# Kernel optimization log

Hardware: AMD Instinct MI355X
Metric: run time of the kernel (lower is better)

The kernel has to match this reference:

```python
import jax, jax.numpy as jnp
import numpy as np

N_NODES = 100000
HIDDEN = 128
E = 524288  # edges per graph (pos and neg)


def setup_inputs() -> dict:
    key = jax.random.key(0)
    ks = jax.random.split(key, 8)
    return {
        "z_src": jax.random.normal(ks[0], (N_NODES, HIDDEN), dtype=jnp.float32),
        "z_dst": jax.random.normal(ks[1], (N_NODES, HIDDEN), dtype=jnp.float32),
        "pos_src": jax.random.randint(ks[2], (E,), 0, N_NODES, dtype=jnp.int64),
        "pos_dst": jax.random.randint(ks[3], (E,), 0, N_NODES, dtype=jnp.int64),
        "neg_src": jax.random.randint(ks[4], (E,), 0, N_NODES, dtype=jnp.int64),
        "neg_dst": jax.random.randint(ks[5], (E,), 0, N_NODES, dtype=jnp.int64),
        "W1": jax.random.normal(ks[6], (2 * HIDDEN, HIDDEN), dtype=jnp.float32) * (1.0 / np.sqrt(2 * HIDDEN)),
        "b1": jnp.zeros((HIDDEN,), dtype=jnp.float32),
        "W2": jax.random.normal(ks[7], (HIDDEN, 1), dtype=jnp.float32) * (1.0 / np.sqrt(HIDDEN)),
        "b2": jnp.zeros((1,), dtype=jnp.float32),
    }


def reference(z_src, z_dst, pos_src, pos_dst, neg_src, neg_dst, W1, b1, W2, b2):
    # Gather endpoint features for pos then neg edges (cat along edge dim)
    src_idx = jnp.concatenate([pos_src, neg_src])  # [2E]
    dst_idx = jnp.concatenate([pos_dst, neg_dst])  # [2E]
    z = jnp.concatenate([z_src[src_idx], z_dst[dst_idx]], axis=-1)  # [2E, 2h]
    z = jax.nn.relu(z @ W1 + b1)  # [2E, h]
    z = z @ W2 + b2               # [2E, 1]
    return z.reshape(-1)
```

## Files before the change

kernel.cpp:

```cpp
#include <hip/hip_runtime.h>
#include <hip/hip_bf16.h>
#include <cstdint>

#define N_NODES 100000
#define HIDDEN  128
#define NEDGE   524288
#define NT      6250
#define PBLK    256
#define WSTRIDE (PBLK * 4)

typedef __attribute__((ext_vector_type(8))) short short8;
typedef __attribute__((ext_vector_type(4))) float f32x4;

__device__ __forceinline__ unsigned short f2b(float f) {
    unsigned u = __float_as_uint(f);
    u += 0x7FFFu + ((u >> 16) & 1u);
    return (unsigned short)(u >> 16);
}
__device__ __forceinline__ float b2f(unsigned x16) {
    return __uint_as_float(x16 << 16);
}

__device__ __forceinline__ void async_copy16(const float* g, float* l) {
    __builtin_amdgcn_global_load_lds(
        (const __attribute__((address_space(1))) unsigned int*)g,
        (__attribute__((address_space(3))) unsigned int*)l,
        16, 0, 0);
}

__global__ void wp_kernel(const float* __restrict__ W1,
                          unsigned short* __restrict__ Wp)
{
    const int f = blockIdx.x;
    const int tb = blockIdx.y;
    const int lane = threadIdx.x;
    const int t = lane & 15, q = lane >> 4;
    const int n = f >> 2, ks = f & 3;
    short8 v;
#pragma unroll
    for (int j = 0; j < 8; ++j)
        v[j] = (short)f2b(W1[(size_t)(tb * 128 + ks * 32 + q * 8 + j) * 128 + n * 16 + t]);
    *(short8*)(Wp + ((size_t)(tb * 32 + f) * 64 + lane) * 8) = v;
}

__global__ __launch_bounds__(256, 2)
void precompute_kernel(const float* __restrict__ z_src,
                       const float* __restrict__ z_dst,
                       const unsigned short* __restrict__ Wp,
                       const float* __restrict__ b1,
                       unsigned short* __restrict__ Asrc,
                       unsigned short* __restrict__ Adst)
{
    const int table = blockIdx.y;
    const float* __restrict__ z = table ? z_dst : z_src;
    unsigned short* __restrict__ A = table ? Adst : Asrc;

    __shared__ float zbuf[4][2][2048];

    const int tid = threadIdx.x;
    const int wave = tid >> 6;
    const int lane = tid & 63;
    const int t = lane & 15;
    const int q = lane >> 4;

    short8 wfrag[32];
    {
        const unsigned short* wp = Wp + ((size_t)table * 32 * 64 + lane) * 8;
#pragma unroll
        for (int f = 0; f < 32; ++f)
            wfrag[f] = *(const short8*)(wp + (size_t)f * 64 * 8);
    }

    float4 b1v[8];
#pragma unroll
    for (int n = 0; n < 8; ++n)
        b1v[n] = (table == 0) ? *(const float4*)(b1 + n * 16 + q * 4)
                              : make_float4(0.f, 0.f, 0.f, 0.f);

    const int lhi = lane >> 5;
    const int llo = lane & 31;
#define STAGE(m0, p)                                                          \
    do {                                                                      \
        _Pragma("unroll")                                                     \
        for (int j = 0; j < 8; ++j) {                                         \
            const int r = j * 2 + lhi;                                        \
            const int c = llo ^ (r & 7);                                      \
            async_copy16(z + (size_t)((m0) + r) * 128 + c * 4,                \
                         &zbuf[wave][p][j * 256]);                            \
        }                                                                     \
    } while (0)

    int tile = blockIdx.x * 4 + wave;
    int p = 0;
    STAGE(tile * 16, 0);
    __builtin_amdgcn_s_waitcnt(0xF70);
    asm volatile("" ::: "memory");

    while (tile < NT) {
        const int m0 = tile * 16;
        const int ntile = tile + WSTRIDE;
        const int nm0 = (ntile < NT ? ntile : tile) * 16;
        STAGE(nm0, p ^ 1);
        asm volatile("" ::: "memory");
        __builtin_amdgcn_s_waitcnt(0xF78);
        asm volatile("" ::: "memory");

        short8 b[4];
#pragma unroll
        for (int ks = 0; ks < 4; ++ks) {
            const int c0 = ks * 8 + 2 * q;
            const int s = t & 7;
            const float4 v0 = *(const float4*)&zbuf[wave][p][(t * 32 + (c0 ^ s)) * 4];
            const float4 v1 = *(const float4*)&zbuf[wave][p][(t * 32 + ((c0 + 1) ^ s)) * 4];
            b[ks][0] = (short)f2b(v0.x); b[ks][1] = (short)f2b(v0.y);
            b[ks][2] = (short)f2b(v0.z); b[ks][3] = (short)f2b(v0.w);
            b[ks][4] = (short)f2b(v1.x); b[ks][5] = (short)f2b(v1.y);
            b[ks][6] = (short)f2b(v1.z); b[ks][7] = (short)f2b(v1.w);
        }

        f32x4 acc[8];
#pragma unroll
        for (int n = 0; n < 8; ++n) acc[n] = (f32x4){0.f, 0.f, 0.f, 0.f};
#pragma unroll
        for (int n = 0; n < 8; ++n)
#pragma unroll
            for (int ks = 0; ks < 4; ++ks)
                acc[n] = __builtin_amdgcn_mfma_f32_16x16x32_bf16(
                             wfrag[n * 4 + ks], b[ks], acc[n], 0, 0, 0);

        unsigned short* ob = (unsigned short*)&zbuf[wave][p][0];
        const int sw = (t & 7) * 2;
#pragma unroll
        for (int n = 0; n < 8; ++n) {
            ushort4 h;
            h.x = f2b(acc[n][0] + b1v[n].x);
            h.y = f2b(acc[n][1] + b1v[n].y);
            h.z = f2b(acc[n][2] + b1v[n].z);
            h.w = f2b(acc[n][3] + b1v[n].w);
            *(ushort4*)&ob[t * 136 + (((n * 4 + q) ^ sw) * 4)] = h;
        }
        const int rr = lane >> 4;
#pragma unroll
        for (int it = 0; it < 4; ++it) {
            const int r = it * 4 + rr;
            const uint4 v = *(const uint4*)&ob[r * 136 + (((2 * t) ^ ((r & 7) * 2)) * 4)];
            *(uint4*)(A + (size_t)(m0 + r) * 128 + t * 8) = v;
        }
        asm volatile("" ::: "memory");

        p ^= 1;
        tile = ntile;
    }
#undef STAGE
}

__global__ __launch_bounds__(256, 6)
void edge_kernel(const unsigned short* __restrict__ Asrc,
                 const unsigned short* __restrict__ Adst,
                 const int* __restrict__ pos_src,
                 const int* __restrict__ pos_dst,
                 const int* __restrict__ neg_src,
                 const int* __restrict__ neg_dst,
                 const float* __restrict__ W2,
                 const float* __restrict__ b2,
                 float* __restrict__ out)
{
    const int tid = threadIdx.x;
    const int t = tid & 15;
    const int g = tid >> 4;

    const bool is_pos = blockIdx.x < 4096;
    const int* __restrict__ sp = is_pos ? pos_src : neg_src;
    const int* __restrict__ dp = is_pos ? pos_dst : neg_dst;
    const int eb = (is_pos ? (int)blockIdx.x : (int)blockIdx.x - 4096) * 128;

    float w2r[8];
#pragma unroll
    for (int j = 0; j < 8; ++j) w2r[j] = W2[t * 8 + j];
    const float bias2 = b2[0];

    int sidx[8], didx[8];
#pragma unroll
    for (int i = 0; i < 8; ++i) {
        sidx[i] = sp[eb + i * 16 + g];
        didx[i] = dp[eb + i * 16 + g];
    }

    uint4 ua[2][2], ub[2][2];
#pragma unroll
    for (int k = 0; k < 2; ++k) {
        ua[0][k] = *(const uint4*)(Asrc + (size_t)sidx[k] * 128 + t * 8);
        ub[0][k] = *(const uint4*)(Adst + (size_t)didx[k] * 128 + t * 8);
    }
    asm volatile("" ::: "memory");

#pragma unroll
    for (int c = 0; c < 4; ++c) {
        if (c < 3) {
#pragma unroll
            for (int k = 0; k < 2; ++k) {
                ua[(c + 1) & 1][k] =
                    *(const uint4*)(Asrc + (size_t)sidx[(c + 1) * 2 + k] * 128 + t * 8);
                ub[(c + 1) & 1][k] =
                    *(const uint4*)(Adst + (size_t)didx[(c + 1) * 2 + k] * 128 + t * 8);
            }
        }
        asm volatile("" ::: "memory");
#pragma unroll
        for (int k = 0; k < 2; ++k) {
            const unsigned* pa = (const unsigned*)&ua[c & 1][k];
            const unsigned* pb = (const unsigned*)&ub[c & 1][k];
            float acc = 0.f;
#pragma unroll
            for (int j2 = 0; j2 < 4; ++j2) {
                float h0 = b2f(pa[j2] & 0xFFFFu) + b2f(pb[j2] & 0xFFFFu);
                float h1 = b2f(pa[j2] >> 16)     + b2f(pb[j2] >> 16);
                h0 = fmaxf(h0, 0.f);
                h1 = fmaxf(h1, 0.f);
                acc = fmaf(h0, w2r[2 * j2], acc);
                acc = fmaf(h1, w2r[2 * j2 + 1], acc);
            }
            acc += __shfl_xor(acc, 1);
            acc += __shfl_xor(acc, 2);
            acc += __shfl_xor(acc, 4);
            acc += __shfl_xor(acc, 8);
            if (t == 0) out[blockIdx.x * 128 + (c * 2 + k) * 16 + g] = acc + bias2;
        }
    }
}

extern "C" void kernel_launch(void* const* d_in, const int* in_sizes, int n_in,
                              void* d_out, int out_size, void* d_ws, size_t ws_size,
                              hipStream_t stream) {
    const float* z_src  = (const float*)d_in[0];
    const float* z_dst  = (const float*)d_in[1];
    const int* pos_src  = (const int*)d_in[2];
    const int* pos_dst  = (const int*)d_in[3];
    const int* neg_src  = (const int*)d_in[4];
    const int* neg_dst  = (const int*)d_in[5];
    const float* W1     = (const float*)d_in[6];
    const float* b1     = (const float*)d_in[7];
    const float* W2     = (const float*)d_in[8];
    const float* b2     = (const float*)d_in[9];
    float* out = (float*)d_out;

    unsigned short* Asrc = (unsigned short*)d_ws;
    unsigned short* Adst = Asrc + (size_t)N_NODES * HIDDEN;
    unsigned short* Wp   = Adst + (size_t)N_NODES * HIDDEN;

    wp_kernel<<<dim3(32, 2), 64, 0, stream>>>(W1, Wp);

    precompute_kernel<<<dim3(PBLK, 2), 256, 0, stream>>>(z_src, z_dst, Wp, b1,
                                                         Asrc, Adst);

    edge_kernel<<<8192, 256, 0, stream>>>(Asrc, Adst, pos_src, pos_dst,
                                          neg_src, neg_dst, W2, b2, out);
}
```

Measured before the change: 219.9 us.

## Issue all edge gathers upfront with staged waitcnt and halve edges per block

The edge kernel now handles 64 edges per block instead of 128, doubling the grid. Each thread issues all four gather loads at once using 32-bit byte offsets and then consumes them in order with explicit vmcnt waits, replacing the two-deep double buffer. The launch bounds occupancy hint rises from 6 to 7. The goal is more memory-level parallelism and cheaper address arithmetic for the random row gathers, at the cost of more blocks and repeated W2 loads per block.

```diff
diff --git a/kernel.cpp b/kernel.cpp
--- a/kernel.cpp
+++ b/kernel.cpp
@@ -154,7 +154,7 @@
 #undef STAGE
 }
 
-__global__ __launch_bounds__(256, 6)
+__global__ __launch_bounds__(256, 7)
 void edge_kernel(const unsigned short* __restrict__ Asrc,
                  const unsigned short* __restrict__ Adst,
                  const int* __restrict__ pos_src,
@@ -169,64 +169,62 @@
     const int t = tid & 15;
     const int g = tid >> 4;
 
-    const bool is_pos = blockIdx.x < 4096;
+    const bool is_pos = blockIdx.x < 8192;
     const int* __restrict__ sp = is_pos ? pos_src : neg_src;
     const int* __restrict__ dp = is_pos ? pos_dst : neg_dst;
-    const int eb = (is_pos ? (int)blockIdx.x : (int)blockIdx.x - 4096) * 128;
+    const int eb = (is_pos ? (int)blockIdx.x : (int)blockIdx.x - 8192) * 64;
 
     float w2r[8];
 #pragma unroll
     for (int j = 0; j < 8; ++j) w2r[j] = W2[t * 8 + j];
     const float bias2 = b2[0];
 
-    int sidx[8], didx[8];
-#pragma unroll
-    for (int i = 0; i < 8; ++i) {
-        sidx[i] = sp[eb + i * 16 + g];
-        didx[i] = dp[eb + i * 16 + g];
-    }
-
-    uint4 ua[2][2], ub[2][2];
-#pragma unroll
-    for (int k = 0; k < 2; ++k) {
-        ua[0][k] = *(const uint4*)(Asrc + (size_t)sidx[k] * 128 + t * 8);
-        ub[0][k] = *(const uint4*)(Adst + (size_t)didx[k] * 128 + t * 8);
+    unsigned soff[4], doff[4];
+#pragma unroll
+    for (int i = 0; i < 4; ++i) {
+        soff[i] = ((unsigned)sp[eb + i * 16 + g] << 8) + t * 16;
+        doff[i] = ((unsigned)dp[eb + i * 16 + g] << 8) + t * 16;
+    }
+
+    const unsigned char* As = (const unsigned char*)Asrc;
+    const unsigned char* Ad = (const unsigned char*)Adst;
+
+    uint4 ua[4], ub[4];
+#pragma unroll
+    for (int i = 0; i < 4; ++i) {
+        ua[i] = *(const uint4*)(As + soff[i]);
+        ub[i] = *(const uint4*)(Ad + doff[i]);
     }
     asm volatile("" ::: "memory");
 
-#pragma unroll
-    for (int c = 0; c < 4; ++c) {
-        if (c < 3) {
-#pragma unroll
-            for (int k = 0; k < 2; ++k) {
-                ua[(c + 1) & 1][k] =
-                    *(const uint4*)(Asrc + (size_t)sidx[(c + 1) * 2 + k] * 128 + t * 8);
-                ub[(c + 1) & 1][k] =
-                    *(const uint4*)(Adst + (size_t)didx[(c + 1) * 2 + k] * 128 + t * 8);
-            }
-        }
-        asm volatile("" ::: "memory");
-#pragma unroll
-        for (int k = 0; k < 2; ++k) {
-            const unsigned* pa = (const unsigned*)&ua[c & 1][k];
-            const unsigned* pb = (const unsigned*)&ub[c & 1][k];
-            float acc = 0.f;
-#pragma unroll
-            for (int j2 = 0; j2 < 4; ++j2) {
-                float h0 = b2f(pa[j2] & 0xFFFFu) + b2f(pb[j2] & 0xFFFFu);
-                float h1 = b2f(pa[j2] >> 16)     + b2f(pb[j2] >> 16);
-                h0 = fmaxf(h0, 0.f);
-                h1 = fmaxf(h1, 0.f);
-                acc = fmaf(h0, w2r[2 * j2], acc);
-                acc = fmaf(h1, w2r[2 * j2 + 1], acc);
-            }
-            acc += __shfl_xor(acc, 1);
-            acc += __shfl_xor(acc, 2);
-            acc += __shfl_xor(acc, 4);
-            acc += __shfl_xor(acc, 8);
-            if (t == 0) out[blockIdx.x * 128 + (c * 2 + k) * 16 + g] = acc + bias2;
-        }
-    }
+#define CHUNK(i, vm)                                                          \
+    do {                                                                      \
+        __builtin_amdgcn_s_waitcnt(0xF70 | (vm));                             \
+        asm volatile("" ::: "memory");                                        \
+        const unsigned* pa = (const unsigned*)&ua[i];                         \
+        const unsigned* pb = (const unsigned*)&ub[i];                         \
+        float acc = 0.f;                                                      \
+        _Pragma("unroll")                                                     \
+        for (int j2 = 0; j2 < 4; ++j2) {                                      \
+            float h0 = b2f(pa[j2] & 0xFFFFu) + b2f(pb[j2] & 0xFFFFu);         \
+            float h1 = b2f(pa[j2] >> 16)     + b2f(pb[j2] >> 16);             \
+            h0 = fmaxf(h0, 0.f);                                              \
+            h1 = fmaxf(h1, 0.f);                                              \
+            acc = fmaf(h0, w2r[2 * j2], acc);                                 \
+            acc = fmaf(h1, w2r[2 * j2 + 1], acc);                             \
+        }                                                                     \
+        acc += __shfl_xor(acc, 1);                                            \
+        acc += __shfl_xor(acc, 2);                                            \
+        acc += __shfl_xor(acc, 4);                                            \
+        acc += __shfl_xor(acc, 8);                                            \
+        if (t == 0) out[blockIdx.x * 64 + (i) * 16 + g] = acc + bias2;        \
+    } while (0)
+
+    CHUNK(0, 6);
+    CHUNK(1, 4);
+    CHUNK(2, 2);
+    CHUNK(3, 0);
+#undef CHUNK
 }
 
 extern "C" void kernel_launch(void* const* d_in, const int* in_sizes, int n_in,
@@ -253,6 +251,6 @@
     precompute_kernel<<<dim3(PBLK, 2), 256, 0, stream>>>(z_src, z_dst, Wp, b1,
                                                          Asrc, Adst);
 
-    edge_kernel<<<8192, 256, 0, stream>>>(Asrc, Adst, pos_src, pos_dst,
-                                          neg_src, neg_dst, W2, b2, out);
-}
+    edge_kernel<<<16384, 256, 0, stream>>>(Asrc, Adst, pos_src, pos_dst,
+                                           neg_src, neg_dst, W2, b2, out);
+}
```

After: 220.9 us. About the same (+0.5%).
